# Kernel optimization log

Hardware: AMD Instinct MI355X
Metric: run time of the kernel (lower is better)

The kernel has to match this reference:

```python
import jax, jax.numpy as jnp
import numpy as np

INPUT_DIM = 128
HIDDEN = 128
OUT = 64
N_LAYERS = 2
HYPER_H = 1024
N_OBJ = 3
TOTAL_PARAMS = INPUT_DIM * HIDDEN + HIDDEN + N_LAYERS * (HIDDEN * HIDDEN + HIDDEN) + HIDDEN * OUT + OUT  # 57792


def setup_inputs() -> dict:
    key = jax.random.key(0)
    ks = jax.random.split(key, 8)
    B = 2048
    x = jax.random.normal(ks[0], (B, INPUT_DIM), dtype=jnp.float32)
    objective_weights = jax.random.uniform(ks[1], (B, N_OBJ), dtype=jnp.float32)
    # hyper MLP params (Linear: y = x @ W.T + b -> store as [in, out] for jnp)
    W1 = jax.random.normal(ks[2], (N_OBJ, HYPER_H), dtype=jnp.float32) * 0.05
    b1 = jnp.zeros((HYPER_H,), dtype=jnp.float32)
    W2 = jax.random.normal(ks[3], (HYPER_H, HYPER_H), dtype=jnp.float32) * 0.03
    b2 = jnp.zeros((HYPER_H,), dtype=jnp.float32)
    W3 = jax.random.normal(ks[4], (HYPER_H, TOTAL_PARAMS), dtype=jnp.float32) * 0.02
    b3 = jnp.zeros((TOTAL_PARAMS,), dtype=jnp.float32)
    return {"x": x, "objective_weights": objective_weights,
            "W1": W1, "b1": b1, "W2": W2, "b2": b2, "W3": W3, "b3": b3}


def _target_forward(x, flat):
    # Unpack per-sample weights from flat_params [B, TOTAL_PARAMS] and apply
    # the chained batched GEMV + bias + relu, ending in softmax.
    B = flat.shape[0]
    idx = 0

    def take_w(out_dim, in_dim):
        nonlocal idx
        w = flat[:, idx:idx + out_dim * in_dim].reshape(B, out_dim, in_dim)
        idx += out_dim * in_dim
        return w

    def take_b(out_dim):
        nonlocal idx
        b = flat[:, idx:idx + out_dim]
        idx += out_dim
        return b

    def linear(w, b, h):
        # per-sample GEMV: [B,o,i] @ [B,i] -> [B,o]
        return jnp.einsum('boi,bi->bo', w, h) + b

    h = jax.nn.relu(linear(take_w(HIDDEN, INPUT_DIM), take_b(HIDDEN), x))
    for _ in range(N_LAYERS):
        h = jax.nn.relu(linear(take_w(HIDDEN, HIDDEN), take_b(HIDDEN), h))
    logits = linear(take_w(OUT, HIDDEN), take_b(OUT), h)
    return jax.nn.softmax(logits, axis=-1)


def reference(x, objective_weights, W1, b1, W2, b2, W3, b3):
    h = jax.nn.relu(objective_weights @ W1 + b1)
    h = jax.nn.relu(h @ W2 + b2)
    flat = h @ W3 + b3  # [B, TOTAL_PARAMS]
    return _target_forward(x, flat)
```

## Files before the change

### kernel.cpp

```cpp
#include <hip/hip_runtime.h>
#include <cstdint>
#include <cstddef>


typedef __attribute__((ext_vector_type(8))) short short8;
typedef __attribute__((ext_vector_type(4))) float f32x4;

__device__ __forceinline__ unsigned short f2bf(float f) {
  union { float f; uint32_t u; } c; c.f = f;
  uint32_t u = c.u;
  return (unsigned short)((u + 0x7FFFu + ((u >> 16) & 1u)) >> 16);
}
__device__ __forceinline__ float bf2f(unsigned short b) {
  union { uint32_t u; float f; } c; c.u = ((uint32_t)b) << 16;
  return c.f;
}
__device__ __forceinline__ int mapbias(int j) {
  if (j < 128) return 16384 + j;
  if (j < 256) return 32768 + j;
  if (j < 384) return 49152 + j;
  return 57344 + j;
}
__device__ __forceinline__ void swz_block(int& bx, int& by) {
  int gx = gridDim.x;
  int n = gx * gridDim.y;
  int f = by * gx + bx;
  int per = n >> 3;
  int s = (f & 7) * per + (f >> 3);
  bx = s % gx; by = s / gx;
}
__device__ __forceinline__ void gl_lds16(const void* g, void* l) {
  __builtin_amdgcn_global_load_lds(
      (const __attribute__((address_space(1))) void*)g,
      (__attribute__((address_space(3))) void*)l, 16, 0, 0);
}

__global__ void prep_x(const float* __restrict__ x, unsigned short* __restrict__ xbf) {
  int i = (blockIdx.x * 256 + threadIdx.x) * 4;
  float4 v = *(const float4*)(x + i);
  ushort4 o; o.x = f2bf(v.x); o.y = f2bf(v.y); o.z = f2bf(v.z); o.w = f2bf(v.w);
  *(ushort4*)(xbf + i) = o;
}

__global__ void hyper1_k(const float* __restrict__ ow, const float* __restrict__ W1,
                         const float* __restrict__ b1, unsigned short* __restrict__ h1bf) {
  int idx = blockIdx.x * 256 + threadIdx.x;
  int b = idx >> 10, j = idx & 1023;
  float s = b1[j] + ow[b * 3 + 0] * W1[j]
                  + ow[b * 3 + 1] * W1[1024 + j]
                  + ow[b * 3 + 2] * W1[2048 + j];
  h1bf[idx] = f2bf(fmaxf(s, 0.f));
}

__global__ void pack_b(const float* __restrict__ src, unsigned short* __restrict__ dst, int N) {
  int idx = blockIdx.x * 256 + threadIdx.x;
  int c = idx % N;
  int g = idx / N;
  int k0 = (g >> 2) * 32 + (g & 3) * 8;
  const float* s = src + (size_t)k0 * N + c;
  uint4 wv;
  wv.x = f2bf(s[0])            | ((uint32_t)f2bf(s[(size_t)N])     << 16);
  wv.y = f2bf(s[2 * (size_t)N]) | ((uint32_t)f2bf(s[3 * (size_t)N]) << 16);
  wv.z = f2bf(s[4 * (size_t)N]) | ((uint32_t)f2bf(s[5 * (size_t)N]) << 16);
  wv.w = f2bf(s[6 * (size_t)N]) | ((uint32_t)f2bf(s[7 * (size_t)N]) << 16);
  *(uint4*)(dst + (size_t)idx * 8) = wv;
}

template <int CMAP, bool RELU, bool OUTBF>
__global__ __launch_bounds__(256, 4)
void gemm_packed(const unsigned short* __restrict__ A, const unsigned short* __restrict__ BP,
                 const float* __restrict__ bias, void* __restrict__ Out,
                 int lda, int ldbp, int ldo, int K) {
  __shared__ __align__(16) char smem[8192];
  char* As = smem;
  char* Bs = smem + 4096;
  int bx = blockIdx.x, by = blockIdx.y;
  swz_block(bx, by);
  int t = threadIdx.x, lane = t & 63, w = t >> 6;
  int lo = lane & 15, hi = lane >> 4;
  int bbase = bx * 64, nbase = by * 64;
  int ar = t >> 2, ach = t & 3;
  int bkg = t >> 6, bc = t & 63;
  int bj = nbase + bc;
  int bcol = (CMAP == 0) ? bj : mapbias(bj);

  f32x4 acc[4] = {};

  for (int kb = 0; kb < K; kb += 32) {
    gl_lds16(A + (size_t)(bbase + ar) * lda + kb + ((ach ^ ((ar >> 1) & 3)) << 3),
             As + t * 16);
    gl_lds16(BP + ((size_t)((kb >> 5) * 4 + bkg) * ldbp + bcol) * 8, Bs + t * 16);
    __syncthreads();
    short8 af[4];
#pragma unroll
    for (int m = 0; m < 4; m++) {
      int row = m * 16 + lo;
      af[m] = *(const short8*)(As + row * 64 + ((hi ^ ((row >> 1) & 3)) << 4));
    }
    short8 bv = *(const short8*)(Bs + (hi * 64 + w * 16 + lo) * 16);
#pragma unroll
    for (int m = 0; m < 4; m++)
      acc[m] = __builtin_amdgcn_mfma_f32_16x16x32_bf16(af[m], bv, acc[m], 0, 0, 0);
    __syncthreads();
  }

  int col = nbase + w * 16 + lo;
  int mc = (CMAP == 0) ? col : mapbias(col);
  float bvadd = bias[mc];
#pragma unroll
  for (int m = 0; m < 4; m++) {
#pragma unroll
    for (int r = 0; r < 4; r++) {
      int row = bbase + m * 16 + hi * 4 + r;
      float v = acc[m][r] + bvadd;
      if (RELU) v = fmaxf(v, 0.f);
      if (OUTBF) ((unsigned short*)Out)[(size_t)row * ldo + col] = f2bf(v);
      else       ((float*)Out)[(size_t)row * ldo + col] = v;
    }
  }
}

template <bool RELU, bool OUTF32>
__global__ __launch_bounds__(512, 4)
void layer_packed(const unsigned short* __restrict__ h2bf,
                  const unsigned short* __restrict__ W3S,
                  const float* __restrict__ b3,
                  const unsigned short* __restrict__ xin,
                  const float* __restrict__ tb, int tbBase,
                  void* __restrict__ Out, int Woff) {
  __shared__ __align__(16) char smem[49152];
  char* As = smem;
  char* Bs = smem + 16384;
  int bx = blockIdx.x, by = blockIdx.y;
  swz_block(bx, by);
  int t = threadIdx.x, lane = t & 63, w = t >> 6;
  int lo = lane & 15, hi = lane >> 4;
  int wm = w >> 1, wo = w & 1;
  int bbase = bx * 128;
  int obase = by * 2;
  int colstart = Woff + obase * 128;

  f32x4 acc[2][8] = {};

  for (int kb = 0; kb < 1024; kb += 64) {
#pragma unroll
    for (int r = 0; r < 2; r++) {
      int idx = r * 512 + t;
      int ar = idx >> 3, ach = idx & 7;
      gl_lds16(h2bf + (size_t)(bbase + ar) * 1024 + kb + ((ach ^ (ar & 7)) << 3),
               As + idx * 16);
    }
    const unsigned short* bsrc = W3S + ((size_t)(kb >> 5) * 4 * 57792 + colstart) * 8;
#pragma unroll
    for (int r = 0; r < 4; r++) {
      int idx = r * 512 + t;
      int kgrp = idx >> 8, c = idx & 255;
      gl_lds16(bsrc + ((size_t)kgrp * 57792 + c) * 8, Bs + idx * 16);
    }
    __syncthreads();
#pragma unroll
    for (int s = 0; s < 2; s++) {
      short8 af[2];
#pragma unroll
      for (int m = 0; m < 2; m++) {
        int row = wm * 32 + m * 16 + lo;
        int pos = (s * 4 + hi) ^ (row & 7);
        af[m] = *(const short8*)(As + row * 128 + (pos << 4));
      }
#pragma unroll
      for (int nf = 0; nf < 8; nf++) {
        short8 bv = *(const short8*)(Bs + (((s * 4 + hi) * 256) + wo * 128 + nf * 16 + lo) * 16);
        acc[0][nf] = __builtin_amdgcn_mfma_f32_16x16x32_bf16(af[0], bv, acc[0][nf], 0, 0, 0);
        acc[1][nf] = __builtin_amdgcn_mfma_f32_16x16x32_bf16(af[1], bv, acc[1][nf], 0, 0, 0);
      }
    }
    __syncthreads();
  }

#pragma unroll
  for (int r = 0; r < 4; r++) {
    int idx = r * 512 + t;
    int row = idx >> 4, ch = idx & 15;
    gl_lds16(xin + (size_t)(bbase + row) * 128 + ch * 8, smem + idx * 16);
  }
  __syncthreads();
  const unsigned short* Xs = (const unsigned short*)smem;

  int o = obase + wo;
  float b3g[8];
#pragma unroll
  for (int nf = 0; nf < 8; nf++) b3g[nf] = b3[colstart + wo * 128 + nf * 16 + lo];

#pragma unroll
  for (int m = 0; m < 2; m++) {
#pragma unroll
    for (int r = 0; r < 4; r++) {
      int brow = wm * 32 + m * 16 + hi * 4 + r;
      float s = 0.f;
#pragma unroll
      for (int nf = 0; nf < 8; nf++) {
        float xv = bf2f(Xs[brow * 128 + nf * 16 + lo]);
        s += (acc[m][nf][r] + b3g[nf]) * xv;
      }
      s += __shfl_xor(s, 1);
      s += __shfl_xor(s, 2);
      s += __shfl_xor(s, 4);
      s += __shfl_xor(s, 8);
      if (lo == 0) {
        int gb = bbase + brow;
        float y = s + tb[(size_t)gb * 448 + tbBase + o];
        if (RELU) y = fmaxf(y, 0.f);
        if (OUTF32) ((float*)Out)[(size_t)gb * 64 + o] = y;
        else        ((unsigned short*)Out)[(size_t)gb * 128 + o] = f2bf(y);
      }
    }
  }
}

template <int CMAP, bool RELU, bool OUTBF>
__global__ __launch_bounds__(256, 2)
void gemm_small(const unsigned short* __restrict__ A, const float* __restrict__ Bsrc,
                const float* __restrict__ bias, void* __restrict__ Out,
                int lda, int ldb, int ldo, int K) {
  __shared__ __align__(16) char smem[8192];
  char* As = smem;
  char* Bs = smem + 4096;
  int bx = blockIdx.x, by = blockIdx.y;
  swz_block(bx, by);
  int t = threadIdx.x, lane = t & 63, w = t >> 6;
  int lo = lane & 15, hi = lane >> 4;
  int bbase = bx * 64, nbase = by * 64;
  int bn = t & 63, bp = t >> 6;
  int bj = nbase + bn;
  int bcol = (CMAP == 0) ? bj : mapbias(bj);
  int ar = t >> 2, ach = t & 3;
  f32x4 acc[4] = {};
  for (int kb = 0; kb < K; kb += 32) {
    uint4 av = *(const uint4*)(A + (size_t)(bbase + ar) * lda + kb + ach * 8);
    *(uint4*)(As + ar * 64 + ((ach ^ (ar & 3)) << 4)) = av;
    float fb[8];
    const float* src = Bsrc + (size_t)(kb + bp * 8) * ldb + bcol;
#pragma unroll
    for (int j = 0; j < 8; j++) fb[j] = src[(size_t)j * ldb];
    uint4 wv;
    wv.x = f2bf(fb[0]) | ((uint32_t)f2bf(fb[1]) << 16);
    wv.y = f2bf(fb[2]) | ((uint32_t)f2bf(fb[3]) << 16);
    wv.z = f2bf(fb[4]) | ((uint32_t)f2bf(fb[5]) << 16);
    wv.w = f2bf(fb[6]) | ((uint32_t)f2bf(fb[7]) << 16);
    *(uint4*)(Bs + bp * 1024 + bn * 16) = wv;
    __syncthreads();
    short8 af[4];
#pragma unroll
    for (int m = 0; m < 4; m++) {
      int row = m * 16 + lo;
      af[m] = *(const short8*)(As + row * 64 + ((hi ^ (row & 3)) << 4));
    }
    short8 bv = *(const short8*)(Bs + hi * 1024 + (w * 16 + lo) * 16);
#pragma unroll
    for (int m = 0; m < 4; m++)
      acc[m] = __builtin_amdgcn_mfma_f32_16x16x32_bf16(af[m], bv, acc[m], 0, 0, 0);
    __syncthreads();
  }
  int col = nbase + w * 16 + lo;
  int mc = (CMAP == 0) ? col : mapbias(col);
  float bvadd = bias[mc];
#pragma unroll
  for (int m = 0; m < 4; m++) {
#pragma unroll
    for (int r = 0; r < 4; r++) {
      int row = bbase + m * 16 + hi * 4 + r;
      float v = acc[m][r] + bvadd;
      if (RELU) v = fmaxf(v, 0.f);
      if (OUTBF) ((unsigned short*)Out)[(size_t)row * ldo + col] = f2bf(v);
      else       ((float*)Out)[(size_t)row * ldo + col] = v;
    }
  }
}

template <bool RELU, bool OUTF32>
__global__ __launch_bounds__(512, 2)
void layer_fused(const unsigned short* __restrict__ h2bf, const float* __restrict__ W3,
                 const float* __restrict__ b3, const unsigned short* __restrict__ xin,
                 const float* __restrict__ tb, int tbBase, void* __restrict__ Out,
                 int Woff) {
  __shared__ __align__(16) char smem[40960];
  char* As = smem;
  char* Bs = smem + 8192;
  int bx = blockIdx.x, by = blockIdx.y;
  swz_block(bx, by);
  int t = threadIdx.x, lane = t & 63, w = t >> 6;
  int lo = lane & 15, hi = lane >> 4;
  int wm = w >> 2, wo = w & 3;
  int bbase = bx * 128;
  int obase = by * 4;
  int o = obase + wo;
  int colstart = Woff + obase * 128;
  int ar = t >> 2, ach = t & 3;
  const float* bcol0 = W3 + colstart + t;
  f32x4 acc[4][8] = {};
  for (int kb = 0; kb < 1024; kb += 32) {
    uint4 av = *(const uint4*)(h2bf + (size_t)(bbase + ar) * 1024 + kb + ach * 8);
    *(uint4*)(As + ar * 64 + ((ach ^ (ar & 3)) << 4)) = av;
#pragma unroll
    for (int p = 0; p < 2; p++) {
      float fb[16];
      const float* src = bcol0 + (size_t)(kb + p * 16) * 57792;
#pragma unroll
      for (int j = 0; j < 16; j++) fb[j] = src[(size_t)j * 57792];
#pragma unroll
      for (int q = 0; q < 2; q++) {
        uint4 wv;
        wv.x = f2bf(fb[q * 8 + 0]) | ((uint32_t)f2bf(fb[q * 8 + 1]) << 16);
        wv.y = f2bf(fb[q * 8 + 2]) | ((uint32_t)f2bf(fb[q * 8 + 3]) << 16);
        wv.z = f2bf(fb[q * 8 + 4]) | ((uint32_t)f2bf(fb[q * 8 + 5]) << 16);
        wv.w = f2bf(fb[q * 8 + 6]) | ((uint32_t)f2bf(fb[q * 8 + 7]) << 16);
        *(uint4*)(Bs + (p * 2 + q) * 8192 + t * 16) = wv;
      }
    }
    __syncthreads();
    short8 af[4];
#pragma unroll
    for (int m = 0; m < 4; m++) {
      int row = wm * 64 + m * 16 + lo;
      af[m] = *(const short8*)(As + row * 64 + ((hi ^ (row & 3)) << 4));
    }
#pragma unroll
    for (int nf = 0; nf < 8; nf++) {
      short8 bv = *(const short8*)(Bs + hi * 8192 + (wo * 128 + nf * 16 + lo) * 16);
#pragma unroll
      for (int m = 0; m < 4; m++)
        acc[m][nf] = __builtin_amdgcn_mfma_f32_16x16x32_bf16(af[m], bv, acc[m][nf], 0, 0, 0);
    }
    __syncthreads();
  }
#pragma unroll
  for (int pass = 0; pass < 4; pass++) {
    int idx = pass * 512 + t;
    int row = idx >> 4, ch = idx & 15;
    uint4 v = *(const uint4*)(xin + (size_t)(bbase + row) * 128 + ch * 8);
    *(uint4*)(Bs + row * 256 + ch * 16) = v;
  }
  __syncthreads();
  const unsigned short* Xs = (const unsigned short*)Bs;
  float b3g[8];
#pragma unroll
  for (int nf = 0; nf < 8; nf++) b3g[nf] = b3[colstart + wo * 128 + nf * 16 + lo];
  float osum[4][4] = {};
#pragma unroll
  for (int m = 0; m < 4; m++) {
#pragma unroll
    for (int r = 0; r < 4; r++) {
      int brow = wm * 64 + m * 16 + hi * 4 + r;
      float s = 0.f;
#pragma unroll
      for (int nf = 0; nf < 8; nf++) {
        float xv = bf2f(Xs[brow * 128 + nf * 16 + lo]);
        s += (acc[m][nf][r] + b3g[nf]) * xv;
      }
      osum[m][r] = s;
    }
  }
#pragma unroll
  for (int m = 0; m < 4; m++) {
#pragma unroll
    for (int r = 0; r < 4; r++) {
      float v = osum[m][r];
      v += __shfl_xor(v, 1);
      v += __shfl_xor(v, 2);
      v += __shfl_xor(v, 4);
      v += __shfl_xor(v, 8);
      if (lo == 0) {
        int brow = wm * 64 + m * 16 + hi * 4 + r;
        int gb = bbase + brow;
        float y = v + tb[(size_t)gb * 448 + tbBase + o];
        if (RELU) y = fmaxf(y, 0.f);
        if (OUTF32) ((float*)Out)[(size_t)gb * 64 + o] = y;
        else        ((unsigned short*)Out)[(size_t)gb * 128 + o] = f2bf(y);
      }
    }
  }
}

__global__ void softmax_k(const float* __restrict__ logits, float* __restrict__ out) {
  int t = threadIdx.x, w = t >> 6, lane = t & 63;
  int row = blockIdx.x * 4 + w;
  float v = logits[row * 64 + lane];
  float m = v;
  m = fmaxf(m, __shfl_xor(m, 1));
  m = fmaxf(m, __shfl_xor(m, 2));
  m = fmaxf(m, __shfl_xor(m, 4));
  m = fmaxf(m, __shfl_xor(m, 8));
  m = fmaxf(m, __shfl_xor(m, 16));
  m = fmaxf(m, __shfl_xor(m, 32));
  float e = expf(v - m);
  float s = e;
  s += __shfl_xor(s, 1);
  s += __shfl_xor(s, 2);
  s += __shfl_xor(s, 4);
  s += __shfl_xor(s, 8);
  s += __shfl_xor(s, 16);
  s += __shfl_xor(s, 32);
  out[row * 64 + lane] = e / s;
}

extern "C" void kernel_launch(void* const* d_in, const int* in_sizes, int n_in,
                              void* d_out, int out_size, void* d_ws, size_t ws_size,
                              hipStream_t stream) {
  (void)in_sizes; (void)n_in; (void)out_size;
  const float* x  = (const float*)d_in[0];
  const float* ow = (const float*)d_in[1];
  const float* W1 = (const float*)d_in[2];
  const float* b1 = (const float*)d_in[3];
  const float* W2 = (const float*)d_in[4];
  const float* b2 = (const float*)d_in[5];
  const float* W3 = (const float*)d_in[6];
  const float* b3 = (const float*)d_in[7];

  char* ws = (char*)d_ws;
  unsigned short* xbf  = (unsigned short*)(ws + 0);
  unsigned short* h1bf = (unsigned short*)(ws + 524288);
  unsigned short* h2bf = (unsigned short*)(ws + 4718592);
  float*          tb   = (float*)(ws + 8912896);
  unsigned short* ht1  = (unsigned short*)(ws + 12582912);
  unsigned short* ht2  = (unsigned short*)(ws + 13107200);
  unsigned short* ht3  = (unsigned short*)(ws + 13631488);
  float*       logits  = (float*)(ws + 14155776);
  unsigned short* W2S  = (unsigned short*)(ws + 14680064);
  unsigned short* W3S  = (unsigned short*)(ws + 16777216);
  const size_t NEED = 16777216 + (size_t)57792 * 1024 * 2;
  float* out = (float*)d_out;

  prep_x<<<256, 256, 0, stream>>>(x, xbf);
  hyper1_k<<<8192, 256, 0, stream>>>(ow, W1, b1, h1bf);

  if (ws_size >= NEED) {
    pack_b<<<512, 256, 0, stream>>>(W2, W2S, 1024);
    gemm_packed<0, true, true><<<dim3(32, 16), 256, 0, stream>>>(h1bf, W2S, b2, h2bf, 1024, 1024, 1024, 1024);
    pack_b<<<28896, 256, 0, stream>>>(W3, W3S, 57792);
    gemm_packed<1, false, false><<<dim3(32, 7), 256, 0, stream>>>(h2bf, W3S, b3, tb, 1024, 57792, 448, 1024);
    layer_packed<true,  false><<<dim3(16, 64), 512, 0, stream>>>(h2bf, W3S, b3, xbf, tb, 0,   ht1, 0);
    layer_packed<true,  false><<<dim3(16, 64), 512, 0, stream>>>(h2bf, W3S, b3, ht1, tb, 128, ht2, 16512);
    layer_packed<true,  false><<<dim3(16, 64), 512, 0, stream>>>(h2bf, W3S, b3, ht2, tb, 256, ht3, 33024);
    layer_packed<false, true ><<<dim3(16, 32), 512, 0, stream>>>(h2bf, W3S, b3, ht3, tb, 384, logits, 49536);
  } else {
    gemm_small<0, true, true><<<dim3(32, 16), 256, 0, stream>>>(h1bf, W2, b2, h2bf, 1024, 1024, 1024, 1024);
    gemm_small<1, false, false><<<dim3(32, 7), 256, 0, stream>>>(h2bf, W3, b3, tb, 1024, 57792, 448, 1024);
    layer_fused<true,  false><<<dim3(16, 32), 512, 0, stream>>>(h2bf, W3, b3, xbf, tb, 0,   ht1, 0);
    layer_fused<true,  false><<<dim3(16, 32), 512, 0, stream>>>(h2bf, W3, b3, ht1, tb, 128, ht2, 16512);
    layer_fused<true,  false><<<dim3(16, 32), 512, 0, stream>>>(h2bf, W3, b3, ht2, tb, 256, ht3, 33024);
    layer_fused<false, true ><<<dim3(16, 16), 512, 0, stream>>>(h2bf, W3, b3, ht3, tb, 384, logits, 49536);
  }
  softmax_k<<<512, 256, 0, stream>>>(logits, out);
}
```

Before: 621.6 us.

## Double-buffer LDS tiles in hyper GEMMs and reorder layer block mapping

Both gemm_packed and layer_packed now use two LDS buffers, so the next K-slice is fetched with global_load_lds while MFMAs run on the current one. layer_packed drops from a 64-wide to a 32-wide K step per stage, with a matching A swizzle. It also maps blocks so consecutive blocks on each XCD share column tiles of W3S, aiming for better L2 reuse. The cost is a smaller K step with more barriers per K in the layer kernel, and double the LDS for gemm_packed.

```diff
diff --git a/kernel.cpp b/kernel.cpp
--- a/kernel.cpp
+++ b/kernel.cpp
@@ -28,6 +28,13 @@
   int per = n >> 3;
   int s = (f & 7) * per + (f >> 3);
   bx = s % gx; by = s / gx;
+}
+__device__ __forceinline__ void swz_bymajor(int& bx, int& by) {
+  int l = blockIdx.y * gridDim.x + blockIdx.x;
+  int xcd = l & 7, rest = l >> 3;
+  int gy8 = gridDim.y >> 3;
+  by = (rest % gy8) * 8 + xcd;
+  bx = rest / gy8;
 }
 __device__ __forceinline__ void gl_lds16(const void* g, void* l) {
   __builtin_amdgcn_global_load_lds(
@@ -71,9 +78,9 @@
 void gemm_packed(const unsigned short* __restrict__ A, const unsigned short* __restrict__ BP,
                  const float* __restrict__ bias, void* __restrict__ Out,
                  int lda, int ldbp, int ldo, int K) {
-  __shared__ __align__(16) char smem[8192];
-  char* As = smem;
-  char* Bs = smem + 4096;
+  __shared__ __align__(16) char smem[16384];
+  char* A0 = smem;         char* B0 = smem + 4096;
+  char* A1 = smem + 8192;  char* B1 = smem + 12288;
   int bx = blockIdx.x, by = blockIdx.y;
   swz_block(bx, by);
   int t = threadIdx.x, lane = t & 63, w = t >> 6;
@@ -86,21 +93,33 @@
 
   f32x4 acc[4] = {};
 
-  for (int kb = 0; kb < K; kb += 32) {
-    gl_lds16(A + (size_t)(bbase + ar) * lda + kb + ((ach ^ ((ar >> 1) & 3)) << 3),
-             As + t * 16);
-    gl_lds16(BP + ((size_t)((kb >> 5) * 4 + bkg) * ldbp + bcol) * 8, Bs + t * 16);
-    __syncthreads();
+  auto stage = [&](int ks, char* Ab, char* Bb) {
+    gl_lds16(A + (size_t)(bbase + ar) * lda + ks * 32 + ((ach ^ ((ar >> 1) & 3)) << 3),
+             Ab + t * 16);
+    gl_lds16(BP + ((size_t)(ks * 4 + bkg) * ldbp + bcol) * 8, Bb + t * 16);
+  };
+  auto comp = [&](char* Ab, char* Bb) {
     short8 af[4];
 #pragma unroll
     for (int m = 0; m < 4; m++) {
       int row = m * 16 + lo;
-      af[m] = *(const short8*)(As + row * 64 + ((hi ^ ((row >> 1) & 3)) << 4));
-    }
-    short8 bv = *(const short8*)(Bs + (hi * 64 + w * 16 + lo) * 16);
+      af[m] = *(const short8*)(Ab + row * 64 + ((hi ^ ((row >> 1) & 3)) << 4));
+    }
+    short8 bv = *(const short8*)(Bb + (hi * 64 + w * 16 + lo) * 16);
 #pragma unroll
     for (int m = 0; m < 4; m++)
       acc[m] = __builtin_amdgcn_mfma_f32_16x16x32_bf16(af[m], bv, acc[m], 0, 0, 0);
+  };
+
+  int NT = K >> 5;
+  stage(0, A0, B0);
+  __syncthreads();
+  for (int ks = 0; ks < NT; ks += 2) {
+    stage(ks + 1, A1, B1);
+    comp(A0, B0);
+    __syncthreads();
+    if (ks + 2 < NT) stage(ks + 2, A0, B0);
+    comp(A1, B1);
     __syncthreads();
   }
 
@@ -129,51 +148,54 @@
                   const float* __restrict__ tb, int tbBase,
                   void* __restrict__ Out, int Woff) {
   __shared__ __align__(16) char smem[49152];
-  char* As = smem;
-  char* Bs = smem + 16384;
-  int bx = blockIdx.x, by = blockIdx.y;
-  swz_block(bx, by);
+  char* A0 = smem;          char* B0 = smem + 8192;
+  char* A1 = smem + 24576;  char* B1 = smem + 32768;
+  int bx, by;
+  swz_bymajor(bx, by);
   int t = threadIdx.x, lane = t & 63, w = t >> 6;
   int lo = lane & 15, hi = lane >> 4;
   int wm = w >> 1, wo = w & 1;
   int bbase = bx * 128;
   int obase = by * 2;
   int colstart = Woff + obase * 128;
+  int ar = t >> 2, ach = t & 3;
 
   f32x4 acc[2][8] = {};
 
-  for (int kb = 0; kb < 1024; kb += 64) {
+  auto stage = [&](int ks, char* Ab, char* Bb) {
+    gl_lds16(h2bf + (size_t)(bbase + ar) * 1024 + ks * 32 + ((ach ^ ((ar >> 1) & 3)) << 3),
+             Ab + t * 16);
 #pragma unroll
     for (int r = 0; r < 2; r++) {
       int idx = r * 512 + t;
-      int ar = idx >> 3, ach = idx & 7;
-      gl_lds16(h2bf + (size_t)(bbase + ar) * 1024 + kb + ((ach ^ (ar & 7)) << 3),
-               As + idx * 16);
-    }
-    const unsigned short* bsrc = W3S + ((size_t)(kb >> 5) * 4 * 57792 + colstart) * 8;
-#pragma unroll
-    for (int r = 0; r < 4; r++) {
-      int idx = r * 512 + t;
       int kgrp = idx >> 8, c = idx & 255;
-      gl_lds16(bsrc + ((size_t)kgrp * 57792 + c) * 8, Bs + idx * 16);
-    }
-    __syncthreads();
-#pragma unroll
-    for (int s = 0; s < 2; s++) {
-      short8 af[2];
-#pragma unroll
-      for (int m = 0; m < 2; m++) {
-        int row = wm * 32 + m * 16 + lo;
-        int pos = (s * 4 + hi) ^ (row & 7);
-        af[m] = *(const short8*)(As + row * 128 + (pos << 4));
-      }
-#pragma unroll
-      for (int nf = 0; nf < 8; nf++) {
-        short8 bv = *(const short8*)(Bs + (((s * 4 + hi) * 256) + wo * 128 + nf * 16 + lo) * 16);
-        acc[0][nf] = __builtin_amdgcn_mfma_f32_16x16x32_bf16(af[0], bv, acc[0][nf], 0, 0, 0);
-        acc[1][nf] = __builtin_amdgcn_mfma_f32_16x16x32_bf16(af[1], bv, acc[1][nf], 0, 0, 0);
-      }
-    }
+      gl_lds16(W3S + ((size_t)(ks * 4 + kgrp) * 57792 + colstart + c) * 8,
+               Bb + idx * 16);
+    }
+  };
+  auto comp = [&](char* Ab, char* Bb) {
+    short8 af[2];
+#pragma unroll
+    for (int m = 0; m < 2; m++) {
+      int row = wm * 32 + m * 16 + lo;
+      af[m] = *(const short8*)(Ab + row * 64 + ((hi ^ ((row >> 1) & 3)) << 4));
+    }
+#pragma unroll
+    for (int nf = 0; nf < 8; nf++) {
+      short8 bv = *(const short8*)(Bb + (hi * 256 + wo * 128 + nf * 16 + lo) * 16);
+      acc[0][nf] = __builtin_amdgcn_mfma_f32_16x16x32_bf16(af[0], bv, acc[0][nf], 0, 0, 0);
+      acc[1][nf] = __builtin_amdgcn_mfma_f32_16x16x32_bf16(af[1], bv, acc[1][nf], 0, 0, 0);
+    }
+  };
+
+  stage(0, A0, B0);
+  __syncthreads();
+  for (int ks = 0; ks < 32; ks += 2) {
+    stage(ks + 1, A1, B1);
+    comp(A0, B0);
+    __syncthreads();
+    if (ks + 2 < 32) stage(ks + 2, A0, B0);
+    comp(A1, B1);
     __syncthreads();
   }
 
```

Result: faster. 606.8 us (-2.4%).
